# Kernel optimization log

Hardware: AMD Instinct MI355X
Metric: run time of the kernel (lower is better)

The kernel has to match this reference:

```python
import jax, jax.numpy as jnp
import numpy as np

ATTACK_RATE = 0.03

def setup_inputs() -> dict:
    key = jax.random.key(0)
    rec_audio = jax.random.normal(key, (256, 131072), dtype=jnp.float32)
    return {"rec_audio": rec_audio}

def reference(rec_audio):
    B, N = rec_audio.shape
    k = int(ATTACK_RATE * N)  # number of samples zeroed per row (without replacement)
    # Gumbel-trick style: per-row uniform scores; top-k scores pick k distinct indices,
    # equivalent to np.random.choice(replace=False) per row, fully vectorized.
    u = jax.random.uniform(jax.random.key(42), (B, N), dtype=jnp.float32)
    _, idx = jax.lax.top_k(u, k)                  # [B, k] distinct indices per row
    rows = jnp.arange(B)[:, None]                 # [B, 1]
    mask = jnp.ones((B, N), dtype=rec_audio.dtype).at[rows, idx].set(0.0)
    return rec_audio * mask
```

## Files before the change

### kernel.cpp

```cpp
#include <hip/hip_runtime.h>
#include <stdint.h>

#define NROWS 256
#define NCOLS 131072
#define KSEL  3932
#define TPB   1024
#define BINS  8192
#define MAXC  512

__device__ __forceinline__ uint32_t rotl32(uint32_t v, int r) {
    return (v << r) | (v >> (32 - r));
}

__device__ __forceinline__ uint32_t jax_bits(uint32_t j) {
    const uint32_t ks0 = 0u;
    const uint32_t ks1 = 42u;
    const uint32_t ks2 = ks0 ^ ks1 ^ 0x1BD11BDAu;
    uint32_t x0 = 0u + ks0;
    uint32_t x1 = j + ks1;
#define TF_RND(r) { x0 += x1; x1 = rotl32(x1, r); x1 ^= x0; }
    TF_RND(13) TF_RND(15) TF_RND(26) TF_RND(6)
    x0 += ks1; x1 += ks2 + 1u;
    TF_RND(17) TF_RND(29) TF_RND(16) TF_RND(24)
    x0 += ks2; x1 += ks0 + 2u;
    TF_RND(13) TF_RND(15) TF_RND(26) TF_RND(6)
    x0 += ks0; x1 += ks1 + 3u;
    TF_RND(17) TF_RND(29) TF_RND(16) TF_RND(24)
    x0 += ks1; x1 += ks2 + 4u;
    TF_RND(13) TF_RND(15) TF_RND(26) TF_RND(6)
    x0 += ks2; x1 += ks0 + 5u;
#undef TF_RND
    return x0 ^ x1;
}

__global__ __launch_bounds__(TPB) void topk_mask_kernel(const float* __restrict__ in,
                                                        float* __restrict__ out) {
    __shared__ uint32_t hist[BINS];
    __shared__ uint32_t chunk[TPB];
    __shared__ uint32_t ckeys[MAXC];
    __shared__ uint32_t s_ccount;
    __shared__ uint32_t s_bstar;
    __shared__ uint32_t s_r;
    __shared__ uint32_t s_tkey;

    const uint32_t row  = blockIdx.x;
    const uint32_t tid  = threadIdx.x;
    const uint32_t base = row * (uint32_t)NCOLS;

    for (uint32_t i = tid; i < BINS; i += TPB) hist[i] = 0u;
    if (tid == 0) s_ccount = 0u;
    __syncthreads();

    for (int it = 0; it < NCOLS / (TPB * 4); ++it) {
        uint32_t c = (uint32_t)it * (TPB * 4) + tid * 4;
        #pragma unroll
        for (int e = 0; e < 4; ++e) {
            uint32_t bits = jax_bits(base + c + e);
            atomicAdd(&hist[bits >> 19], 1u);
        }
    }
    __syncthreads();

    uint32_t cs = 0;
    #pragma unroll
    for (int b = 0; b < BINS / TPB; ++b) cs += hist[tid * (BINS / TPB) + b];
    chunk[tid] = cs;
    __syncthreads();

    uint32_t S = cs;
    for (uint32_t off = 1; off < TPB; off <<= 1) {
        uint32_t v = (tid + off < TPB) ? chunk[tid + off] : 0u;
        __syncthreads();
        S += v;
        chunk[tid] = S;
        __syncthreads();
    }

    const uint32_t above = S - cs;
    if (above < KSEL && S >= KSEL) {
        uint32_t acc = above;
        for (int b = BINS / TPB - 1; b >= 0; --b) {
            uint32_t bin = tid * (BINS / TPB) + b;
            uint32_t h = hist[bin];
            if (acc < KSEL && acc + h >= KSEL) {
                s_bstar = bin;
                s_r = KSEL - acc;
            }
            acc += h;
        }
    }
    __syncthreads();

    const uint32_t bstar = s_bstar;
    const uint32_t r     = s_r;

    const float4* in4  = (const float4*)(in + base);
    float4*       out4 = (float4*)(out + base);
    for (int it = 0; it < NCOLS / (TPB * 4); ++it) {
        uint32_t vi = (uint32_t)it * TPB + tid;
        uint32_t c  = vi * 4;
        float4 v = in4[vi];
        float* pv = (float*)&v;
        #pragma unroll
        for (int e = 0; e < 4; ++e) {
            uint32_t bits = jax_bits(base + c + e);
            uint32_t bin = bits >> 19;
            if (bin > bstar) {
                pv[e] = 0.0f;
            } else if (bin == bstar) {
                uint32_t key = (((bits >> 9) & 1023u) << 17) | (131071u - (c + e));
                uint32_t pos = atomicAdd(&s_ccount, 1u);
                if (pos < MAXC) ckeys[pos] = key;
            }
        }
        out4[vi] = v;
    }
    __syncthreads();

    uint32_t cc = s_ccount; if (cc > MAXC) cc = MAXC;
    if (tid < cc) {
        uint32_t mykey = ckeys[tid];
        uint32_t rank = 0;
        for (uint32_t i = 0; i < cc; ++i) rank += (ckeys[i] > mykey) ? 1u : 0u;
        if (rank == r - 1) s_tkey = mykey;
    }
    __syncthreads();

    const uint32_t tkey = s_tkey;

    if (tid < cc) {
        uint32_t mykey = ckeys[tid];
        if (mykey >= tkey) {
            uint32_t c = 131071u - (mykey & 0x1FFFFu);
            out[base + c] = 0.0f;
        }
    }
}

extern "C" void kernel_launch(void* const* d_in, const int* in_sizes, int n_in,
                              void* d_out, int out_size, void* d_ws, size_t ws_size,
                              hipStream_t stream) {
    const float* in = (const float*)d_in[0];
    float* out = (float*)d_out;
    hipLaunchKernelGGL(topk_mask_kernel, dim3(NROWS), dim3(TPB), 0, stream, in, out);
}
```

Measured before the change: 337.5 us.

## Cache packed 8-bit bins in registers and avoid recomputing Threefry in mask pass

The histogram pass now bins on the top 8 bits (256 bins) and keeps each element's bin byte packed in registers. The mask pass reuses those bytes instead of recomputing the Threefry hash for every element, so the random-bit generation is paid once rather than twice. The full hash is recomputed only for the candidates in the boundary bin, and their keys are built from that. The coarser bins make the boundary bin hold about 512 candidates on average, so MAXC is raised to 1024; a heavier bin would overflow and give wrong results. Rotations use alignbit and the loops are fully unrolled, which raises register pressure.

```diff
diff --git a/kernel.cpp b/kernel.cpp
--- a/kernel.cpp
+++ b/kernel.cpp
@@ -5,11 +5,12 @@
 #define NCOLS 131072
 #define KSEL  3932
 #define TPB   1024
-#define BINS  8192
-#define MAXC  512
+#define VITERS (NCOLS / (TPB * 4))
+#define BINS  256
+#define MAXC  1024
 
 __device__ __forceinline__ uint32_t rotl32(uint32_t v, int r) {
-    return (v << r) | (v >> (32 - r));
+    return __builtin_amdgcn_alignbit(v, v, 32 - r);
 }
 
 __device__ __forceinline__ uint32_t jax_bits(uint32_t j) {
@@ -36,7 +37,7 @@
 __global__ __launch_bounds__(TPB) void topk_mask_kernel(const float* __restrict__ in,
                                                         float* __restrict__ out) {
     __shared__ uint32_t hist[BINS];
-    __shared__ uint32_t chunk[TPB];
+    __shared__ uint32_t scanb[BINS];
     __shared__ uint32_t ckeys[MAXC];
     __shared__ uint32_t s_ccount;
     __shared__ uint32_t s_bstar;
@@ -47,46 +48,44 @@
     const uint32_t tid  = threadIdx.x;
     const uint32_t base = row * (uint32_t)NCOLS;
 
-    for (uint32_t i = tid; i < BINS; i += TPB) hist[i] = 0u;
+    uint32_t pk[VITERS];
+
+    if (tid < BINS) hist[tid] = 0u;
     if (tid == 0) s_ccount = 0u;
     __syncthreads();
 
-    for (int it = 0; it < NCOLS / (TPB * 4); ++it) {
-        uint32_t c = (uint32_t)it * (TPB * 4) + tid * 4;
-        #pragma unroll
-        for (int e = 0; e < 4; ++e) {
-            uint32_t bits = jax_bits(base + c + e);
-            atomicAdd(&hist[bits >> 19], 1u);
-        }
+    #pragma unroll
+    for (int it = 0; it < VITERS; ++it) {
+        uint32_t vi = (uint32_t)it * TPB + tid;
+        uint32_t j  = base + vi * 4u;
+        uint32_t b0 = jax_bits(j + 0u);
+        uint32_t b1 = jax_bits(j + 1u);
+        uint32_t b2 = jax_bits(j + 2u);
+        uint32_t b3 = jax_bits(j + 3u);
+        atomicAdd(&hist[b0 >> 24], 1u);
+        atomicAdd(&hist[b1 >> 24], 1u);
+        atomicAdd(&hist[b2 >> 24], 1u);
+        atomicAdd(&hist[b3 >> 24], 1u);
+        pk[it] = (b0 >> 24) | ((b1 >> 24) << 8) | ((b2 >> 24) << 16) | ((b3 >> 24) << 24);
     }
     __syncthreads();
 
-    uint32_t cs = 0;
-    #pragma unroll
-    for (int b = 0; b < BINS / TPB; ++b) cs += hist[tid * (BINS / TPB) + b];
-    chunk[tid] = cs;
+    uint32_t h = 0, S = 0;
+    if (tid < BINS) { h = hist[tid]; scanb[tid] = h; }
     __syncthreads();
-
-    uint32_t S = cs;
-    for (uint32_t off = 1; off < TPB; off <<= 1) {
-        uint32_t v = (tid + off < TPB) ? chunk[tid + off] : 0u;
+    S = h;
+    for (uint32_t off = 1; off < BINS; off <<= 1) {
+        uint32_t v = 0;
+        if (tid < BINS && tid + off < BINS) v = scanb[tid + off];
         __syncthreads();
-        S += v;
-        chunk[tid] = S;
+        if (tid < BINS) { S += v; scanb[tid] = S; }
         __syncthreads();
     }
-
-    const uint32_t above = S - cs;
-    if (above < KSEL && S >= KSEL) {
-        uint32_t acc = above;
-        for (int b = BINS / TPB - 1; b >= 0; --b) {
-            uint32_t bin = tid * (BINS / TPB) + b;
-            uint32_t h = hist[bin];
-            if (acc < KSEL && acc + h >= KSEL) {
-                s_bstar = bin;
-                s_r = KSEL - acc;
-            }
-            acc += h;
+    if (tid < BINS) {
+        uint32_t above = S - h;
+        if (above < KSEL && S >= KSEL) {
+            s_bstar = tid;
+            s_r = KSEL - above;
         }
     }
     __syncthreads();
@@ -96,21 +95,21 @@
 
     const float4* in4  = (const float4*)(in + base);
     float4*       out4 = (float4*)(out + base);
-    for (int it = 0; it < NCOLS / (TPB * 4); ++it) {
+    #pragma unroll
+    for (int it = 0; it < VITERS; ++it) {
         uint32_t vi = (uint32_t)it * TPB + tid;
-        uint32_t c  = vi * 4;
+        uint32_t c  = vi * 4u;
         float4 v = in4[vi];
+        uint32_t p = pk[it];
         float* pv = (float*)&v;
         #pragma unroll
         for (int e = 0; e < 4; ++e) {
-            uint32_t bits = jax_bits(base + c + e);
-            uint32_t bin = bits >> 19;
+            uint32_t bin = (p >> (8 * e)) & 0xFFu;
             if (bin > bstar) {
                 pv[e] = 0.0f;
             } else if (bin == bstar) {
-                uint32_t key = (((bits >> 9) & 1023u) << 17) | (131071u - (c + e));
                 uint32_t pos = atomicAdd(&s_ccount, 1u);
-                if (pos < MAXC) ckeys[pos] = key;
+                if (pos < MAXC) ckeys[pos] = c + (uint32_t)e;
             }
         }
         out4[vi] = v;
@@ -118,22 +117,25 @@
     __syncthreads();
 
     uint32_t cc = s_ccount; if (cc > MAXC) cc = MAXC;
+    uint32_t mykey = 0, myc = 0;
     if (tid < cc) {
-        uint32_t mykey = ckeys[tid];
+        myc = ckeys[tid];
+        uint32_t bits = jax_bits(base + myc);
+        mykey = (((bits >> 9) & 0x7FFFu) << 17) | (131071u - myc);
+    }
+    __syncthreads();
+    if (tid < cc) ckeys[tid] = mykey;
+    __syncthreads();
+
+    if (tid < cc) {
         uint32_t rank = 0;
         for (uint32_t i = 0; i < cc; ++i) rank += (ckeys[i] > mykey) ? 1u : 0u;
         if (rank == r - 1) s_tkey = mykey;
     }
     __syncthreads();
 
-    const uint32_t tkey = s_tkey;
-
-    if (tid < cc) {
-        uint32_t mykey = ckeys[tid];
-        if (mykey >= tkey) {
-            uint32_t c = 131071u - (mykey & 0x1FFFFu);
-            out[base + c] = 0.0f;
-        }
+    if (tid < cc && mykey >= s_tkey) {
+        out[base + myc] = 0.0f;
     }
 }
 
```

Result: faster. 309.1 us (-8.4%).
